# Performance work log

Hardware: AMD Instinct MI355X
Metric: run time of the kernel (lower is better)

## Reference

```python
import jax, jax.numpy as jnp
import numpy as np

LAYERS, STACKS = 10, 4
DILATIONS = [2 ** l for _ in range(STACKS) for l in range(LAYERS)]  # 40 blocks


def setup_inputs() -> dict:
    key = jax.random.key(0)
    ks = jax.random.split(key, 7)
    B, C, L, SC, NB = 4, 64, 8192, 256, len(DILATIONS)
    scale = 0.05  # keep 40 stacked residual blocks numerically tame
    return {
        "x": jax.random.normal(ks[0], (B, C, L), dtype=jnp.float32),
        "dc_w": jax.random.normal(ks[1], (NB, C, C, 2), dtype=jnp.float32) * scale,
        "dc_b": jax.random.normal(ks[2], (NB, C), dtype=jnp.float32) * scale,
        "conv_w": jax.random.normal(ks[3], (NB, C, C), dtype=jnp.float32) * scale,
        "conv_b": jax.random.normal(ks[4], (NB, C), dtype=jnp.float32) * scale,
        "skip_w": jax.random.normal(ks[5], (NB, SC, C), dtype=jnp.float32) * scale,
        "skip_b": jax.random.normal(ks[6], (NB, SC), dtype=jnp.float32) * scale,
        "skip_size": 4096,
    }


def reference(x, dc_w, dc_b, conv_w, conv_b, skip_w, skip_b, skip_size):
    # x: [B, res_ch, L]; returns stacked skips [n_blocks, B, skip_ch, skip_size]
    out = x
    skips = []
    for i, d in enumerate(DILATIONS):
        h = (jnp.einsum('oi,bil->bol', dc_w[i, :, :, 0], out[:, :, :-d])
             + jnp.einsum('oi,bil->bol', dc_w[i, :, :, 1], out[:, :, d:])
             + dc_b[i][None, :, None])
        g = jax.nn.relu(h)
        r = jnp.einsum('oi,bil->bol', conv_w[i], g) + conv_b[i][None, :, None]
        out = r + out[:, :, -r.shape[2]:]  # residual on aligned (last) timesteps
        s = jnp.einsum('oi,bil->bol', skip_w[i], g) + skip_b[i][None, :, None]
        skips.append(s[:, :, -skip_size:])
    return jnp.stack(skips)
```

## Files before the change

kernel.cpp:

```cpp
#include <hip/hip_runtime.h>


#define CC    64
#define SCC   256
#define BB    4
#define LL0   8192
#define NBLK  40
#define SKIPN 4096

typedef __attribute__((ext_vector_type(8))) short bf16x8;
typedef __attribute__((ext_vector_type(4))) float f32x4;
typedef unsigned short us;

__device__ __forceinline__ us f2bf(float f) {
    union { float f; unsigned u; } v; v.f = f;
    return (us)((v.u + 0x7FFF + ((v.u >> 16) & 1)) >> 16);
}
__device__ __forceinline__ unsigned pk2(float a, float b) {
    return (unsigned)f2bf(a) | ((unsigned)f2bf(b) << 16);
}
__device__ __forceinline__ uint2 pk4(f32x4 v) {
    return (uint2){pk2(v[0], v[1]), pk2(v[2], v[3])};
}
__device__ __forceinline__ int sws(int r, int c) {
    return (r << 6) + ((((c >> 3) ^ r) & 7) << 3) + (c & 7);
}
__device__ __forceinline__ int swh(int r, int c) {
    return (r << 6) + ((((c >> 3) ^ r) & 7) << 3) + (c & 7);
}
__device__ __forceinline__ int scb(int s, int chunk) {
    return (s << 6) + (((chunk ^ (s & 7)) & 7) << 3);
}

__global__ __launch_bounds__(256) void prep_kernel(
    const float* __restrict__ x, float* __restrict__ xt_out,
    const float* __restrict__ dc_w, const float* __restrict__ conv_w,
    const float* __restrict__ skip_w,
    us* __restrict__ wcat, us* __restrict__ cwb, us* __restrict__ swb)
{
    if (blockIdx.x < 512) {
        __shared__ float tile[64][65];
        const int b = blockIdx.x >> 7, t0 = (blockIdx.x & 127) * 64;
        const int tid = threadIdx.x;
        #pragma unroll
        for (int p = 0; p < 4; ++p) {
            const int c = p * 16 + (tid >> 4), j = tid & 15;
            const float4 v = *(const float4*)(x + ((size_t)b * CC + c) * LL0 + t0 + j * 4);
            tile[c][j*4+0]=v.x; tile[c][j*4+1]=v.y; tile[c][j*4+2]=v.z; tile[c][j*4+3]=v.w;
        }
        __syncthreads();
        #pragma unroll
        for (int p = 0; p < 4; ++p) {
            const int r = p * 16 + (tid >> 4), h = tid & 15;
            float4 v = {tile[h*4+0][r], tile[h*4+1][r], tile[h*4+2][r], tile[h*4+3][r]};
            *(float4*)(xt_out + ((size_t)b * LL0 + t0 + r) * CC + h * 4) = v;
        }
        return;
    }
    const int n_sw = NBLK * SCC * CC, n_cw = NBLK * CC * CC, n_wc = NBLK * CC * 128;
    for (int idx = (blockIdx.x - 512) * blockDim.x + threadIdx.x; idx < n_sw;
         idx += 1024 * blockDim.x) {
        swb[idx] = f2bf(skip_w[idx]);
        if (idx < n_cw) cwb[idx] = f2bf(conv_w[idx]);
        if (idx < n_wc) {
            const int i = idx >> 13, o = (idx >> 7) & 63, kk = idx & 127;
            wcat[idx] = f2bf(dc_w[(((i * CC + o) * CC) + (kk & 63)) * 2 + (kk >> 6)]);
        }
    }
}

__device__ __forceinline__ void skip_body8(
    int e, int blk0,
    const us* __restrict__ g_all, const us* __restrict__ swb,
    const float* __restrict__ skip_b, float* __restrict__ out)
{
    constexpr int ROWS = 128;
    constexpr int TPB = (SKIPN / ROWS) * BB;
    const int tid = threadIdx.x, lane = tid & 63, wv = tid >> 6;
    const int j = blk0 + e / TPB;
    const int id = e % TPB;
    const int tt = id % (SKIPN / ROWS);
    const int b  = id / (SKIPN / ROWS);
    const us* g  = g_all + ((size_t)j * BB + b) * SKIPN * CC;
    const us* sw = swb + (size_t)j * SCC * CC;
    const float* sb = skip_b + j * SCC;
    float* op = out + ((size_t)j * BB + b) * SCC * SKIPN;

    const int trow = tt * ROWS + wv * 16 + (lane & 15);
    bf16x8 a[2];
    a[0] = *(const bf16x8*)(g + (size_t)trow * CC + (lane >> 4) * 8);
    a[1] = *(const bf16x8*)(g + (size_t)trow * CC + 32 + (lane >> 4) * 8);
    const int tstore = tt * ROWS + wv * 16 + ((lane >> 4) << 2);
    #pragma unroll 4
    for (int n = 0; n < 16; ++n) {
        const int sc = n * 16 + (lane & 15);
        const float bias = sb[sc];
        f32x4 acc = (f32x4){bias, bias, bias, bias};
        const us* wrow = sw + sc * CC + (lane >> 4) * 8;
        acc = __builtin_amdgcn_mfma_f32_16x16x32_bf16(a[0], *(const bf16x8*)(wrow), acc, 0, 0, 0);
        acc = __builtin_amdgcn_mfma_f32_16x16x32_bf16(a[1], *(const bf16x8*)(wrow + 32), acc, 0, 0, 0);
        *(float4*)(op + (size_t)sc * SKIPN + tstore) = (float4){acc[0], acc[1], acc[2], acc[3]};
    }
}

__global__ __launch_bounds__(512) void fused6_kernel(
    const float* __restrict__ cur, float* __restrict__ nxt,
    const us* __restrict__ wcat_all, const us* __restrict__ cwb_all,
    const float* __restrict__ db_all, const float* __restrict__ cb_all,
    us* __restrict__ g_all, int blk0, int Lin, int ntiles,
    const us* __restrict__ swb, const float* __restrict__ skip_b,
    float* __restrict__ out, int pb0)
{
    const int wg = blockIdx.x, chain = BB * ntiles;
    if (wg >= chain) { skip_body8(wg - chain, pb0, g_all, swb, skip_b, out); return; }

    constexpr int TOUT = 96, R0 = 159, RCAP = 160;
    __shared__ __align__(16) float sm[RCAP * CC];
    __shared__ __align__(16) us  smb[RCAP * CC];
    __shared__ __align__(16) us  scr[8 * 16 * CC];

    const int tid = threadIdx.x, lane = tid & 63, wv = tid >> 6;
    const int b = wg / ntiles, t0 = (wg % ntiles) * TOUT;
    const float* src = cur + (size_t)b * LL0 * CC;
    const int s = lane & 15, q = lane >> 4;
    us* myscr = scr + wv * (16 * CC);

    for (int base = 0; base < R0; base += 32) {
        const int row = base + (tid >> 4);
        const int h4 = (tid & 15) * 4;
        if (row < R0) {
            int gt = t0 + row; if (gt > Lin - 1) gt = Lin - 1;
            f32x4 v = *(const f32x4*)(src + (size_t)gt * CC + h4);
            *(f32x4*)(sm + sws(row, h4)) = v;
            *(uint2*)(smb + swh(row, h4)) = pk4(v);
        }
    }
    __syncthreads();

    int Rcur = R0, Lj = Lin;
    for (int j = 0; j < 6; ++j) {
        const int d = 1 << j;
        const int Rn = Rcur - d;
        Lj -= d;
        const us* wj = wcat_all + (size_t)(blk0 + j) * CC * 128;
        const us* cj = cwb_all + (size_t)(blk0 + j) * CC * CC;
        const float* dbj = db_all + (blk0 + j) * CC;
        const float* cbj = cb_all + (blk0 + j) * CC;
        const int wbase = Lj - SKIPN;
        us* gdst = g_all + ((size_t)(blk0 + j) * BB + b) * SKIPN * CC;

        f32x4 r2[2][4];
        #pragma unroll
        for (int fi = 0; fi < 2; ++fi) {
            const int fg = wv + fi * 8;
            if (fg * 16 < Rn) {
                const int t = fg * 16 + s;
                const int tc = t > Rn - 1 ? Rn - 1 : t;
                bf16x8 af0 = *(const bf16x8*)(smb + swh(tc,     q * 8));
                bf16x8 af1 = *(const bf16x8*)(smb + swh(tc,     32 + q * 8));
                bf16x8 af2 = *(const bf16x8*)(smb + swh(tc + d, q * 8));
                bf16x8 af3 = *(const bf16x8*)(smb + swh(tc + d, 32 + q * 8));
                #pragma unroll
                for (int n = 0; n < 4; ++n) {
                    const int o0 = n * 16 + q * 4;
                    f32x4 acc = *(const f32x4*)(dbj + o0);
                    const us* wr = wj + (n * 16 + s) * 128 + q * 8;
                    acc = __builtin_amdgcn_mfma_f32_16x16x32_bf16(*(const bf16x8*)(wr),      af0, acc, 0, 0, 0);
                    acc = __builtin_amdgcn_mfma_f32_16x16x32_bf16(*(const bf16x8*)(wr + 32), af1, acc, 0, 0, 0);
                    acc = __builtin_amdgcn_mfma_f32_16x16x32_bf16(*(const bf16x8*)(wr + 64), af2, acc, 0, 0, 0);
                    acc = __builtin_amdgcn_mfma_f32_16x16x32_bf16(*(const bf16x8*)(wr + 96), af3, acc, 0, 0, 0);
                    #pragma unroll
                    for (int r = 0; r < 4; ++r) acc[r] = acc[r] > 0.f ? acc[r] : 0.f;
                    *(uint2*)(myscr + scb(s, n * 2 + (q >> 1)) + (q & 1) * 4) = pk4(acc);
                }
                bf16x8 g0 = *(const bf16x8*)(myscr + scb(s, q));
                bf16x8 g1 = *(const bf16x8*)(myscr + scb(s, 4 + q));
                {
                    const int gt = t0 + t;
                    if (t < Rn && gt >= wbase && gt < Lj) {
                        us* gr = gdst + (size_t)(gt - wbase) * CC;
                        #pragma unroll
                        for (int h = 0; h < 2; ++h) {
                            const int ck = q * 2 + h;
                            *(bf16x8*)(gr + ck * 8) = *(const bf16x8*)(myscr + scb(s, ck));
                        }
                    }
                }
                #pragma unroll
                for (int n = 0; n < 4; ++n) {
                    const int o0 = n * 16 + q * 4;
                    f32x4 r = *(const f32x4*)(cbj + o0);
                    const us* wr = cj + (n * 16 + s) * CC + q * 8;
                    r = __builtin_amdgcn_mfma_f32_16x16x32_bf16(*(const bf16x8*)(wr),      g0, r, 0, 0, 0);
                    r = __builtin_amdgcn_mfma_f32_16x16x32_bf16(*(const bf16x8*)(wr + 32), g1, r, 0, 0, 0);
                    r += *(const f32x4*)(sm + sws(tc + d, o0));
                    r2[fi][n] = r;
                }
            }
        }
        __syncthreads();
        #pragma unroll
        for (int fi = 0; fi < 2; ++fi) {
            const int fg = wv + fi * 8;
            const int t = fg * 16 + s;
            if (t < Rn) {
                #pragma unroll
                for (int n = 0; n < 4; ++n) {
                    const int o0 = n * 16 + q * 4;
                    *(f32x4*)(sm + sws(t, o0)) = r2[fi][n];
                    *(uint2*)(smb + swh(t, o0)) = pk4(r2[fi][n]);
                }
            }
        }
        __syncthreads();
        Rcur = Rn;
    }

    float* dst = nxt + (size_t)b * LL0 * CC;
    for (int base = 0; base < TOUT; base += 32) {
        const int row = base + (tid >> 4);
        const int h4 = (tid & 15) * 4;
        const int gt = t0 + row;
        if (row < TOUT && gt < Lj)
            *(float4*)(dst + (size_t)gt * CC + h4) = *(const float4*)(sm + sws(row, h4));
    }
}

__global__ __launch_bounds__(512) void single_kernel(
    const float* __restrict__ cur, float* __restrict__ nxt,
    const us* __restrict__ wcat, const us* __restrict__ cwb,
    const float* __restrict__ db, const float* __restrict__ cb,
    us* __restrict__ g_out,
    int d, int Lin, int Lout, int ntiles,
    const us* __restrict__ g_all, const us* __restrict__ swb,
    const float* __restrict__ skip_b, float* __restrict__ out, int pb0)
{
    const int wg = blockIdx.x, chain = BB * ntiles;
    if (wg >= chain) { skip_body8(wg - chain, pb0, g_all, swb, skip_b, out); return; }

    __shared__ __align__(16) us   xb0[64 * CC];
    __shared__ __align__(16) us   xb1[64 * CC];
    __shared__ __align__(16) float x1f[64 * CC];
    __shared__ __align__(16) us   scr[8 * 16 * CC];

    const int tid = threadIdx.x, lane = tid & 63, wv = tid >> 6;
    const int b = wg / ntiles, t0 = (wg % ntiles) * 64;
    const float* src = cur + (size_t)b * LL0 * CC;
    const int s = lane & 15, q = lane >> 4;
    us* myscr = scr + wv * (16 * CC);
    const int Lv = (Lout - t0) < 64 ? (Lout - t0) : 64;

    #pragma unroll
    for (int p = 0; p < 2; ++p) {
        const int row = p * 32 + (tid >> 4);
        const int h4 = (tid & 15) * 4;
        int ta = t0 + row;     if (ta > Lin - 1) ta = Lin - 1;
        int tb = t0 + row + d; if (tb > Lin - 1) tb = Lin - 1;
        f32x4 v0 = *(const f32x4*)(src + (size_t)ta * CC + h4);
        f32x4 v1 = *(const f32x4*)(src + (size_t)tb * CC + h4);
        *(uint2*)(xb0 + swh(row, h4)) = pk4(v0);
        *(uint2*)(xb1 + swh(row, h4)) = pk4(v1);
        *(f32x4*)(x1f + sws(row, h4)) = v1;
    }
    __syncthreads();

    const int tl = wv * 16 + s;
    const int tc = tl > Lv - 1 ? Lv - 1 : tl;
    bf16x8 af0 = *(const bf16x8*)(xb0 + swh(tc, q * 8));
    bf16x8 af1 = *(const bf16x8*)(xb0 + swh(tc, 32 + q * 8));
    bf16x8 af2 = *(const bf16x8*)(xb1 + swh(tc, q * 8));
    bf16x8 af3 = *(const bf16x8*)(xb1 + swh(tc, 32 + q * 8));
    #pragma unroll
    for (int n = 0; n < 4; ++n) {
        const int o0 = n * 16 + q * 4;
        f32x4 acc = *(const f32x4*)(db + o0);
        const us* wr = wcat + (n * 16 + s) * 128 + q * 8;
        acc = __builtin_amdgcn_mfma_f32_16x16x32_bf16(*(const bf16x8*)(wr),      af0, acc, 0, 0, 0);
        acc = __builtin_amdgcn_mfma_f32_16x16x32_bf16(*(const bf16x8*)(wr + 32), af1, acc, 0, 0, 0);
        acc = __builtin_amdgcn_mfma_f32_16x16x32_bf16(*(const bf16x8*)(wr + 64), af2, acc, 0, 0, 0);
        acc = __builtin_amdgcn_mfma_f32_16x16x32_bf16(*(const bf16x8*)(wr + 96), af3, acc, 0, 0, 0);
        #pragma unroll
        for (int r = 0; r < 4; ++r) acc[r] = acc[r] > 0.f ? acc[r] : 0.f;
        *(uint2*)(myscr + scb(s, n * 2 + (q >> 1)) + (q & 1) * 4) = pk4(acc);
    }
    bf16x8 g0 = *(const bf16x8*)(myscr + scb(s, q));
    bf16x8 g1 = *(const bf16x8*)(myscr + scb(s, 4 + q));
    {
        const int gt = t0 + tl;
        const int wb = Lout - SKIPN;
        if (tl < Lv && gt >= wb) {
            us* gr = g_out + ((size_t)b * SKIPN + (gt - wb)) * CC;
            #pragma unroll
            for (int h = 0; h < 2; ++h) {
                const int ck = q * 2 + h;
                *(bf16x8*)(gr + ck * 8) = *(const bf16x8*)(myscr + scb(s, ck));
            }
        }
    }
    float* dst = nxt + (size_t)b * LL0 * CC + (size_t)(t0 + tl) * CC;
    #pragma unroll
    for (int n = 0; n < 4; ++n) {
        const int o0 = n * 16 + q * 4;
        f32x4 r = *(const f32x4*)(cb + o0);
        const us* wr = cwb + (n * 16 + s) * CC + q * 8;
        r = __builtin_amdgcn_mfma_f32_16x16x32_bf16(*(const bf16x8*)(wr),      g0, r, 0, 0, 0);
        r = __builtin_amdgcn_mfma_f32_16x16x32_bf16(*(const bf16x8*)(wr + 32), g1, r, 0, 0, 0);
        r += *(const f32x4*)(x1f + sws(tl < 63 ? tl : 63, o0));
        if (tl < Lv) *(f32x4*)(dst + o0) = r;
    }
}

__global__ __launch_bounds__(512) void skip_kernel(
    const us* __restrict__ g_all, const us* __restrict__ swb,
    const float* __restrict__ skip_b, float* __restrict__ out, int blk0)
{
    skip_body8(blockIdx.x, blk0, g_all, swb, skip_b, out);
}

extern "C" void kernel_launch(void* const* d_in, const int* in_sizes, int n_in,
                              void* d_out, int out_size, void* d_ws, size_t ws_size,
                              hipStream_t stream)
{
    const float* x      = (const float*)d_in[0];
    const float* dc_w   = (const float*)d_in[1];
    const float* dc_b   = (const float*)d_in[2];
    const float* conv_w = (const float*)d_in[3];
    const float* conv_b = (const float*)d_in[4];
    const float* skip_w = (const float*)d_in[5];
    const float* skip_b = (const float*)d_in[6];
    float* out = (float*)d_out;

    char* ws = (char*)d_ws;
    float* bufA = (float*)ws;  ws += (size_t)BB * LL0 * CC * 4;
    float* bufB = (float*)ws;  ws += (size_t)BB * LL0 * CC * 4;
    us* g_all = (us*)ws;       ws += (size_t)NBLK * BB * SKIPN * CC * 2;
    us* wcat = (us*)ws;        ws += (size_t)NBLK * CC * 128 * 2;
    us* cwb  = (us*)ws;        ws += (size_t)NBLK * CC * CC * 2;
    us* swb  = (us*)ws;        ws += (size_t)NBLK * SCC * CC * 2;

    prep_kernel<<<1536, 256, 0, stream>>>(x, bufA, dc_w, conv_w, skip_w, wcat, cwb, swb);

    float* bufs[2] = {bufA, bufB};
    const size_t GSZ = (size_t)BB * SKIPN * CC;
    int Lc = LL0, blk = 0, qq = 0, produced = 0, skipped = 0;
    for (int st = 0; st < 4; ++st) {
        {
            const int Lout = Lc - 63;
            const int nt = (Lout + 95) / 96;
            int cap = produced - skipped; if (cap > 4) cap = 4;
            fused6_kernel<<<dim3(BB * nt + cap * 128), 512, 0, stream>>>(
                bufs[qq & 1], bufs[(qq + 1) & 1], wcat, cwb, dc_b, conv_b,
                g_all, blk, Lc, nt, swb, skip_b, out, skipped);
            skipped += cap; produced += 6; blk += 6; Lc = Lout; ++qq;
        }
        for (int dl = 6; dl < 10; ++dl) {
            const int d = 1 << dl;
            const int Lout = Lc - d;
            const int nt = (Lout + 63) / 64;
            int cap = produced - skipped; if (cap > 4) cap = 4;
            single_kernel<<<dim3(BB * nt + cap * 128), 512, 0, stream>>>(
                bufs[qq & 1], bufs[(qq + 1) & 1],
                wcat + (size_t)blk * CC * 128, cwb + (size_t)blk * CC * CC,
                dc_b + blk * CC, conv_b + blk * CC,
                g_all + (size_t)blk * GSZ,
                d, Lc, Lout, nt, g_all, swb, skip_b, out, skipped);
            skipped += cap; produced += 1; blk += 1; Lc = Lout; ++qq;
        }
    }
    const int rem = NBLK - skipped;
    if (rem > 0)
        skip_kernel<<<dim3(rem * 128), 512, 0, stream>>>(g_all, swb, skip_b, out, skipped);
}
```

Before: 854.0 us.

## Rewrite single-layer kernel with smaller 32-step tiles and rebalance skip work

Replaces the 512-thread single-layer kernel with a 256-thread block kernel over 32-timestep tiles. It uses a concatenated swizzled bf16 input tile, splits output channels across wave pairs, and stages g in shared memory. Skip GEMM work is reshaped to 4 waves (64 rows per workgroup), and the skip blocks piggybacked per launch are rebalanced (1 in the fused kernel, 3 in each single-layer launch). The aim is more workgroups and higher occupancy for the small dilated layers. The cost is more grid overhead, scalar strided global stores for the residual output, and a different skip/chain overlap balance.

```diff
diff --git a/kernel.cpp b/kernel.cpp
--- a/kernel.cpp
+++ b/kernel.cpp
@@ -7,6 +7,7 @@
 #define LL0   8192
 #define NBLK  40
 #define SKIPN 4096
+#define TTC   32
 
 typedef __attribute__((ext_vector_type(8))) short bf16x8;
 typedef __attribute__((ext_vector_type(4))) float f32x4;
@@ -27,6 +28,10 @@
 }
 __device__ __forceinline__ int swh(int r, int c) {
     return (r << 6) + ((((c >> 3) ^ r) & 7) << 3) + (c & 7);
+}
+__device__ __forceinline__ int swx(int r, int k) {
+    int ch = k >> 3; ch = (ch & 8) | ((ch ^ r) & 7);
+    return (r << 7) + (ch << 3) + (k & 7);
 }
 __device__ __forceinline__ int scb(int s, int chunk) {
     return (s << 6) + (((chunk ^ (s & 7)) & 7) << 3);
@@ -69,12 +74,13 @@
     }
 }
 
-__device__ __forceinline__ void skip_body8(
+template<int NW>
+__device__ __forceinline__ void skip_body(
     int e, int blk0,
     const us* __restrict__ g_all, const us* __restrict__ swb,
     const float* __restrict__ skip_b, float* __restrict__ out)
 {
-    constexpr int ROWS = 128;
+    constexpr int ROWS = NW * 16;
     constexpr int TPB = (SKIPN / ROWS) * BB;
     const int tid = threadIdx.x, lane = tid & 63, wv = tid >> 6;
     const int j = blk0 + e / TPB;
@@ -112,7 +118,7 @@
     float* __restrict__ out, int pb0)
 {
     const int wg = blockIdx.x, chain = BB * ntiles;
-    if (wg >= chain) { skip_body8(wg - chain, pb0, g_all, swb, skip_b, out); return; }
+    if (wg >= chain) { skip_body<8>(wg - chain, pb0, g_all, swb, skip_b, out); return; }
 
     constexpr int TOUT = 96, R0 = 159, RCAP = 160;
     __shared__ __align__(16) float sm[RCAP * CC];
@@ -226,7 +232,7 @@
     }
 }
 
-__global__ __launch_bounds__(512) void single_kernel(
+__global__ __launch_bounds__(256) void block_kernel(
     const float* __restrict__ cur, float* __restrict__ nxt,
     const us* __restrict__ wcat, const us* __restrict__ cwb,
     const float* __restrict__ db, const float* __restrict__ cb,
@@ -236,85 +242,104 @@
     const float* __restrict__ skip_b, float* __restrict__ out, int pb0)
 {
     const int wg = blockIdx.x, chain = BB * ntiles;
-    if (wg >= chain) { skip_body8(wg - chain, pb0, g_all, swb, skip_b, out); return; }
-
-    __shared__ __align__(16) us   xb0[64 * CC];
-    __shared__ __align__(16) us   xb1[64 * CC];
-    __shared__ __align__(16) float x1f[64 * CC];
-    __shared__ __align__(16) us   scr[8 * 16 * CC];
+    if (wg >= chain) { skip_body<4>(wg - chain, pb0, g_all, swb, skip_b, out); return; }
+
+    __shared__ __align__(16) us xt[TTC * 128];
+    __shared__ __align__(16) us gs[TTC * CC];
+    __shared__ float x1f[CC][TTC + 1];
 
     const int tid = threadIdx.x, lane = tid & 63, wv = tid >> 6;
-    const int b = wg / ntiles, t0 = (wg % ntiles) * 64;
+    const int b = wg / ntiles, t0 = (wg % ntiles) * TTC;
     const float* src = cur + (size_t)b * LL0 * CC;
-    const int s = lane & 15, q = lane >> 4;
-    us* myscr = scr + wv * (16 * CC);
-    const int Lv = (Lout - t0) < 64 ? (Lout - t0) : 64;
 
     #pragma unroll
     for (int p = 0; p < 2; ++p) {
-        const int row = p * 32 + (tid >> 4);
-        const int h4 = (tid & 15) * 4;
+        const int row = p * 16 + (tid >> 4);
+        const int h = tid & 15;
         int ta = t0 + row;     if (ta > Lin - 1) ta = Lin - 1;
         int tb = t0 + row + d; if (tb > Lin - 1) tb = Lin - 1;
-        f32x4 v0 = *(const f32x4*)(src + (size_t)ta * CC + h4);
-        f32x4 v1 = *(const f32x4*)(src + (size_t)tb * CC + h4);
-        *(uint2*)(xb0 + swh(row, h4)) = pk4(v0);
-        *(uint2*)(xb1 + swh(row, h4)) = pk4(v1);
-        *(f32x4*)(x1f + sws(row, h4)) = v1;
+        const float4 v0 = *(const float4*)(src + (size_t)ta * CC + h * 4);
+        const float4 v1 = *(const float4*)(src + (size_t)tb * CC + h * 4);
+        uint2 p0, p1;
+        p0.x = pk2(v0.x, v0.y); p0.y = pk2(v0.z, v0.w);
+        p1.x = pk2(v1.x, v1.y); p1.y = pk2(v1.z, v1.w);
+        *(uint2*)(xt + swx(row, h * 4)) = p0;
+        *(uint2*)(xt + swx(row, 64 + h * 4)) = p1;
+        x1f[h * 4 + 0][row] = v1.x;
+        x1f[h * 4 + 1][row] = v1.y;
+        x1f[h * 4 + 2][row] = v1.z;
+        x1f[h * 4 + 3][row] = v1.w;
     }
     __syncthreads();
 
-    const int tl = wv * 16 + s;
-    const int tc = tl > Lv - 1 ? Lv - 1 : tl;
-    bf16x8 af0 = *(const bf16x8*)(xb0 + swh(tc, q * 8));
-    bf16x8 af1 = *(const bf16x8*)(xb0 + swh(tc, 32 + q * 8));
-    bf16x8 af2 = *(const bf16x8*)(xb1 + swh(tc, q * 8));
-    bf16x8 af3 = *(const bf16x8*)(xb1 + swh(tc, 32 + q * 8));
-    #pragma unroll
-    for (int n = 0; n < 4; ++n) {
-        const int o0 = n * 16 + q * 4;
-        f32x4 acc = *(const f32x4*)(db + o0);
-        const us* wr = wcat + (n * 16 + s) * 128 + q * 8;
-        acc = __builtin_amdgcn_mfma_f32_16x16x32_bf16(*(const bf16x8*)(wr),      af0, acc, 0, 0, 0);
-        acc = __builtin_amdgcn_mfma_f32_16x16x32_bf16(*(const bf16x8*)(wr + 32), af1, acc, 0, 0, 0);
-        acc = __builtin_amdgcn_mfma_f32_16x16x32_bf16(*(const bf16x8*)(wr + 64), af2, acc, 0, 0, 0);
-        acc = __builtin_amdgcn_mfma_f32_16x16x32_bf16(*(const bf16x8*)(wr + 96), af3, acc, 0, 0, 0);
-        #pragma unroll
-        for (int r = 0; r < 4; ++r) acc[r] = acc[r] > 0.f ? acc[r] : 0.f;
-        *(uint2*)(myscr + scb(s, n * 2 + (q >> 1)) + (q & 1) * 4) = pk4(acc);
-    }
-    bf16x8 g0 = *(const bf16x8*)(myscr + scb(s, q));
-    bf16x8 g1 = *(const bf16x8*)(myscr + scb(s, 4 + q));
+    const int rf = wv >> 1, oh = wv & 1;
+    const int row = rf * 16 + (lane & 15);
+
+    bf16x8 a1[4];
+    #pragma unroll
+    for (int ks = 0; ks < 4; ++ks)
+        a1[ks] = *(const bf16x8*)(xt + swx(row, ks * 32 + (lane >> 4) * 8));
+    f32x4 acc[2];
+    #pragma unroll
+    for (int n = 0; n < 2; ++n) {
+        const int o = oh * 32 + n * 16 + (lane & 15);
+        const float bias = db[o];
+        acc[n] = (f32x4){bias, bias, bias, bias};
+        const us* wrow = wcat + o * 128 + (lane >> 4) * 8;
+        #pragma unroll
+        for (int ks = 0; ks < 4; ++ks)
+            acc[n] = __builtin_amdgcn_mfma_f32_16x16x32_bf16(
+                a1[ks], *(const bf16x8*)(wrow + ks * 32), acc[n], 0, 0, 0);
+    }
+    const int wr = rf * 16 + ((lane >> 4) << 2);
+    #pragma unroll
+    for (int n = 0; n < 2; ++n) {
+        const int o = oh * 32 + n * 16 + (lane & 15);
+        #pragma unroll
+        for (int r = 0; r < 4; ++r) {
+            float g = acc[n][r]; g = g > 0.f ? g : 0.f;
+            gs[swh(wr + r, o)] = f2bf(g);
+        }
+    }
+    __syncthreads();
+
+    bf16x8 a2[2];
+    #pragma unroll
+    for (int ks = 0; ks < 2; ++ks)
+        a2[ks] = *(const bf16x8*)(gs + swh(row, ks * 32 + (lane >> 4) * 8));
     {
-        const int gt = t0 + tl;
-        const int wb = Lout - SKIPN;
-        if (tl < Lv && gt >= wb) {
-            us* gr = g_out + ((size_t)b * SKIPN + (gt - wb)) * CC;
+        const int tloc = wr;
+        const int t = t0 + tloc;
+        #pragma unroll
+        for (int n = 0; n < 2; ++n) {
+            const int o = oh * 32 + n * 16 + (lane & 15);
+            const float bias = cb[o];
+            f32x4 racc = (f32x4){bias, bias, bias, bias};
+            const us* wrow = cwb + o * CC + (lane >> 4) * 8;
+            racc = __builtin_amdgcn_mfma_f32_16x16x32_bf16(a2[0], *(const bf16x8*)(wrow), racc, 0, 0, 0);
+            racc = __builtin_amdgcn_mfma_f32_16x16x32_bf16(a2[1], *(const bf16x8*)(wrow + 32), racc, 0, 0, 0);
+            float* outp = nxt + (size_t)b * LL0 * CC + (size_t)t * CC + o;
             #pragma unroll
-            for (int h = 0; h < 2; ++h) {
-                const int ck = q * 2 + h;
-                *(bf16x8*)(gr + ck * 8) = *(const bf16x8*)(myscr + scb(s, ck));
-            }
-        }
-    }
-    float* dst = nxt + (size_t)b * LL0 * CC + (size_t)(t0 + tl) * CC;
-    #pragma unroll
-    for (int n = 0; n < 4; ++n) {
-        const int o0 = n * 16 + q * 4;
-        f32x4 r = *(const f32x4*)(cb + o0);
-        const us* wr = cwb + (n * 16 + s) * CC + q * 8;
-        r = __builtin_amdgcn_mfma_f32_16x16x32_bf16(*(const bf16x8*)(wr),      g0, r, 0, 0, 0);
-        r = __builtin_amdgcn_mfma_f32_16x16x32_bf16(*(const bf16x8*)(wr + 32), g1, r, 0, 0, 0);
-        r += *(const f32x4*)(x1f + sws(tl < 63 ? tl : 63, o0));
-        if (tl < Lv) *(f32x4*)(dst + o0) = r;
-    }
-}
-
-__global__ __launch_bounds__(512) void skip_kernel(
+            for (int r = 0; r < 4; ++r)
+                if (t + r < Lout) outp[(size_t)r * CC] = racc[r] + x1f[o][tloc + r];
+        }
+    }
+
+    {
+        const int row2 = tid >> 3, ch8 = tid & 7;
+        const int gt = t0 + row2;
+        const int wbase = Lout - SKIPN;
+        if (gt >= wbase && gt < Lout)
+            *(bf16x8*)(g_out + ((size_t)b * SKIPN + (gt - wbase)) * CC + ch8 * 8) =
+                *(const bf16x8*)(gs + swh(row2, ch8 * 8));
+    }
+}
+
+__global__ __launch_bounds__(256) void skip_kernel(
     const us* __restrict__ g_all, const us* __restrict__ swb,
     const float* __restrict__ skip_b, float* __restrict__ out, int blk0)
 {
-    skip_body8(blockIdx.x, blk0, g_all, swb, skip_b, out);
+    skip_body<4>(blockIdx.x, blk0, g_all, swb, skip_b, out);
 }
 
 extern "C" void kernel_launch(void* const* d_in, const int* in_sizes, int n_in,
@@ -347,7 +372,7 @@
         {
             const int Lout = Lc - 63;
             const int nt = (Lout + 95) / 96;
-            int cap = produced - skipped; if (cap > 4) cap = 4;
+            int cap = produced - skipped; if (cap > 1) cap = 1;
             fused6_kernel<<<dim3(BB * nt + cap * 128), 512, 0, stream>>>(
                 bufs[qq & 1], bufs[(qq + 1) & 1], wcat, cwb, dc_b, conv_b,
                 g_all, blk, Lc, nt, swb, skip_b, out, skipped);
@@ -356,9 +381,9 @@
         for (int dl = 6; dl < 10; ++dl) {
             const int d = 1 << dl;
             const int Lout = Lc - d;
-            const int nt = (Lout + 63) / 64;
-            int cap = produced - skipped; if (cap > 4) cap = 4;
-            single_kernel<<<dim3(BB * nt + cap * 128), 512, 0, stream>>>(
+            const int nt = (Lout + TTC - 1) / TTC;
+            int cap = produced - skipped; if (cap > 3) cap = 3;
+            block_kernel<<<dim3(BB * nt + cap * 256), 256, 0, stream>>>(
                 bufs[qq & 1], bufs[(qq + 1) & 1],
                 wcat + (size_t)blk * CC * 128, cwb + (size_t)blk * CC * CC,
                 dc_b + blk * CC, conv_b + blk * CC,
@@ -369,5 +394,5 @@
     }
     const int rem = NBLK - skipped;
     if (rem > 0)
-        skip_kernel<<<dim3(rem * 128), 512, 0, stream>>>(g_all, swb, skip_b, out, skipped);
-}
+        skip_kernel<<<dim3(rem * 256), 256, 0, stream>>>(g_all, swb, skip_b, out, skipped);
+}
```

Result: faster. 716.4 us, median of 2 (-16.1%).
